# Kernel optimization log

Hardware: AMD Instinct MI355X
Metric: run time of the kernel (lower is better)

Reference implementation:

```python
import jax, jax.numpy as jnp
import numpy as np
from jax.scipy.special import logsumexp

B, DK, N, M = 16, 512, 1024, 1024
SINKHORN_ITERS = 5
EPS = 1e-8


def setup_inputs() -> dict:
    key = jax.random.key(0)
    k1, k2, k3, k4, k5 = jax.random.split(key, 5)
    return {
        "src_embedding": jax.random.normal(k1, (B, DK, N), dtype=jnp.float32),
        "tgt_embedding": jax.random.normal(k2, (B, DK, M), dtype=jnp.float32),
        "src": jax.random.normal(k3, (B, 3, N), dtype=jnp.float32),
        "tgt": jax.random.normal(k4, (B, 3, M), dtype=jnp.float32),
        # temperature must be positive; uniform in [0.05, 1.0)
        "temperature": jax.random.uniform(k5, (B,), dtype=jnp.float32, minval=0.05, maxval=1.0),
    }


def sinkhorn(scores, n_iters):
    # ZeroPad2d((0,1,0,1)): pad one slack row and one slack column with zeros
    scores = jnp.pad(scores, ((0, 0), (0, 1), (0, 1)))
    for _ in range(n_iters):
        # row normalization (all rows except slack row)
        top = scores[:, :-1, :] - logsumexp(scores[:, :-1, :], axis=2, keepdims=True)
        scores = jnp.concatenate([top, scores[:, -1:, :]], axis=1)
        # column normalization (all cols except slack col)
        left = scores[:, :, :-1] - logsumexp(scores[:, :, :-1], axis=1, keepdims=True)
        scores = jnp.concatenate([left, scores[:, :, -1:]], axis=2)
    return scores[:, :-1, :-1]


def reference(src_embedding, tgt_embedding, src, tgt, temperature):
    b, d_k, n = src_embedding.shape
    # [B, N, M] similarity scores
    dists = jnp.einsum('bdn,bdm->bnm', src_embedding, tgt_embedding) / jnp.sqrt(jnp.float32(d_k))
    affinity = dists / temperature[:, None, None]
    log_perm = sinkhorn(affinity, SINKHORN_ITERS)
    perm = jnp.exp(log_perm)                                             # [B,N,M]
    perm_norm = perm / (jnp.sum(perm, axis=2, keepdims=True) + EPS)      # [B,N,M]
    # soft correspondence: weighted_tgt[b,:,i] = sum_j perm_norm[b,i,j] * tgt[b,:,j]
    weighted_tgt = jnp.einsum('bdm,bnm->bdn', tgt, perm_norm)            # [B,3,N]
    weights = jnp.sum(perm, axis=-1, keepdims=True)                      # [B,N,1]
    weights_norm = weights / (jnp.sum(weights, axis=1, keepdims=True) + EPS)
    weights_norm = jnp.swapaxes(weights_norm, 1, 2)                      # [B,1,N]
    src_centroid = jnp.sum(src * weights_norm, axis=2, keepdims=True)    # [B,3,1]
    tgt_centroid = jnp.sum(weighted_tgt * weights_norm, axis=2, keepdims=True)
    src_centered = src - src_centroid
    corr_centered = (weighted_tgt - tgt_centroid) * weights_norm
    # weighted cross-covariance, batched 3x3
    H = jnp.einsum('bin,bjn->bij', src_centered, corr_centered)          # [B,3,3]
    # batched Procrustes via SVD (torch.svd: H = u diag(s) v^T; jnp: H = u diag(s) vh)
    u, s, vh = jnp.linalg.svd(H)
    v = jnp.swapaxes(vh, 1, 2)
    ut = jnp.swapaxes(u, 1, 2)
    r = jnp.matmul(v, ut)
    r_det = jnp.linalg.det(r)                                            # [B]
    diag = jnp.stack([jnp.ones_like(r_det), jnp.ones_like(r_det), r_det], axis=-1)  # [B,3]
    R = jnp.matmul(v * diag[:, None, :], ut)                             # [B,3,3]
    t = (jnp.matmul(-R, src_centroid) + tgt_centroid).reshape(b, 3)
    return R, t, perm_norm
```

## Files before the change

kernel.cpp:

```cpp
#include <hip/hip_runtime.h>
#include <math.h>

#define BB 16
#define NN 1024
#define MM 1024
#define DKK 512
#define CHUNKS 16

typedef short short8 __attribute__((ext_vector_type(8)));
typedef float f32x4 __attribute__((ext_vector_type(4)));

__device__ float g_u[BB*NN];
__device__ float g_v[BB*MM];
__device__ float g_w[BB*NN];
__device__ float g_wt[BB*3*NN];
__device__ float g_pm[BB*CHUNKS*MM];
__device__ float g_ps[BB*CHUNKS*MM];
__device__ __attribute__((aligned(16))) unsigned short gAh[BB*NN*DKK];
__device__ __attribute__((aligned(16))) unsigned short gAl[BB*NN*DKK];
__device__ __attribute__((aligned(16))) unsigned short gBh[BB*MM*DKK];
__device__ __attribute__((aligned(16))) unsigned short gBl[BB*MM*DKK];

__global__ __launch_bounds__(256) void zero_v_kernel() {
    int i = blockIdx.x*256 + threadIdx.x;
    if (i < BB*MM) g_v[i] = 0.0f;
}

__device__ __forceinline__ unsigned int bf16_rne(float x){
    unsigned int u = __float_as_uint(x);
    return (u + 0x7fffu + ((u>>16)&1u)) >> 16;
}

__global__ __launch_bounds__(256) void convert_split(const float* __restrict__ X,
                                                     int which) {
    unsigned short* Hh = which ? gBh : gAh;
    unsigned short* Hl = which ? gBl : gAl;
    int b  = blockIdx.z;
    int d0 = blockIdx.y * 64;
    int i0 = blockIdx.x * 64;
    __shared__ float T[64*65];
    const float* Xb = X + ((size_t)b*DKK + d0)*NN + i0;
    int t = threadIdx.x;
#pragma unroll
    for (int it=0; it<4; ++it){
        int lin = t + 256*it;
        int d = lin >> 4;
        int i4 = lin & 15;
        float4 v = *(const float4*)(Xb + (size_t)d*NN + i4*4);
        T[(i4*4+0)*65 + d] = v.x;
        T[(i4*4+1)*65 + d] = v.y;
        T[(i4*4+2)*65 + d] = v.z;
        T[(i4*4+3)*65 + d] = v.w;
    }
    __syncthreads();
    size_t obase = ((size_t)b*NN + i0)*DKK + d0;
#pragma unroll
    for (int it=0; it<2; ++it){
        int c = t + 256*it;
        int i = c >> 3;
        int p = c & 7;
        unsigned int hw[4], lw[4];
#pragma unroll
        for (int j=0;j<4;j++){
            float x0 = T[i*65 + p*8 + 2*j];
            float x1 = T[i*65 + p*8 + 2*j+1];
            unsigned int h0 = bf16_rne(x0);
            unsigned int h1 = bf16_rne(x1);
            float hf0 = __uint_as_float(h0<<16);
            float hf1 = __uint_as_float(h1<<16);
            unsigned int l0 = bf16_rne(x0 - hf0);
            unsigned int l1 = bf16_rne(x1 - hf1);
            hw[j] = h0 | (h1<<16);
            lw[j] = l0 | (l1<<16);
        }
        size_t eo = obase + (size_t)i*DKK + p*8;
        uint4 hv; hv.x=hw[0]; hv.y=hw[1]; hv.z=hw[2]; hv.w=hw[3];
        uint4 lv; lv.x=lw[0]; lv.y=lw[1]; lv.z=lw[2]; lv.w=lw[3];
        *(uint4*)(Hh + eo) = hv;
        *(uint4*)(Hl + eo) = lv;
    }
}

__global__ __launch_bounds__(256) void gemm_mfma(const float* __restrict__ temp,
                                                 float* __restrict__ C) {
    int b  = blockIdx.z;
    int i0 = blockIdx.y * 128;
    int j0 = blockIdx.x * 128;
    __shared__ __attribute__((aligned(16))) char lds[40960];
    int t = threadIdx.x;
    int lane = t & 63, w = t >> 6;
    int wr = w >> 1, wc = w & 1;
    const size_t eb = (size_t)b * NN * DKK;
    const uint4* pAh = (const uint4*)(gAh + eb);
    const uint4* pAl = (const uint4*)(gAl + eb);
    const uint4* pBh = (const uint4*)(gBh + eb);
    const uint4* pBl = (const uint4*)(gBl + eb);
    int rr = t >> 2, pp = t & 3;

    f32x4 acc[16];
#pragma unroll
    for (int q=0;q<16;q++) acc[q] = (f32x4){0.f,0.f,0.f,0.f};

    uint4 ra0, ra1, la0, la1, rb0, rb1, lb0, lb1;
    auto loadk = [&](int k0){
        int kq = k0 >> 3;
        ra0 = pAh[(size_t)(i0+rr)*64 + kq + pp];
        ra1 = pAh[(size_t)(i0+rr+64)*64 + kq + pp];
        la0 = pAl[(size_t)(i0+rr)*64 + kq + pp];
        la1 = pAl[(size_t)(i0+rr+64)*64 + kq + pp];
        rb0 = pBh[(size_t)(j0+rr)*64 + kq + pp];
        rb1 = pBh[(size_t)(j0+rr+64)*64 + kq + pp];
        lb0 = pBl[(size_t)(j0+rr)*64 + kq + pp];
        lb1 = pBl[(size_t)(j0+rr+64)*64 + kq + pp];
    };
    loadk(0);

    const char* fa = lds + (wr*64 + (lane&15))*80 + (lane>>4)*16;
    const char* fb = lds + 20480 + (wc*64 + (lane&15))*80 + (lane>>4)*16;
    char* wbase = lds + rr*80 + pp*16;

    for (int ks=0; ks<16; ++ks){
        __syncthreads();
        *(uint4*)(wbase + 0)     = ra0;
        *(uint4*)(wbase + 5120)  = ra1;
        *(uint4*)(wbase + 10240) = la0;
        *(uint4*)(wbase + 15360) = la1;
        *(uint4*)(wbase + 20480) = rb0;
        *(uint4*)(wbase + 25600) = rb1;
        *(uint4*)(wbase + 30720) = lb0;
        *(uint4*)(wbase + 35840) = lb1;
        __syncthreads();
        if (ks+1 < 16) loadk((ks+1)*32);

        short8 ah[4], al[4];
#pragma unroll
        for (int mf=0;mf<4;mf++){
            ah[mf] = *(const short8*)(fa + mf*1280);
            al[mf] = *(const short8*)(fa + 10240 + mf*1280);
        }
#pragma unroll
        for (int nf=0;nf<4;nf++){
            short8 bh = *(const short8*)(fb + nf*1280);
            short8 bl = *(const short8*)(fb + 10240 + nf*1280);
#pragma unroll
            for (int mf=0;mf<4;mf++){
                acc[mf*4+nf] = __builtin_amdgcn_mfma_f32_16x16x32_bf16(ah[mf], bh, acc[mf*4+nf], 0,0,0);
                acc[mf*4+nf] = __builtin_amdgcn_mfma_f32_16x16x32_bf16(ah[mf], bl, acc[mf*4+nf], 0,0,0);
                acc[mf*4+nf] = __builtin_amdgcn_mfma_f32_16x16x32_bf16(al[mf], bh, acc[mf*4+nf], 0,0,0);
            }
        }
    }

    float scale = 1.0f/(22.62741699796952f * temp[b]);
    float* Cb = C + ((size_t)b<<20);
    int r0c = i0 + wr*64 + ((lane>>4)<<2);
    int c0c = j0 + wc*64 + (lane&15);
#pragma unroll
    for (int mf=0;mf<4;mf++){
#pragma unroll
        for (int r2=0;r2<4;r2++){
            float* rowp = Cb + (size_t)(r0c + mf*16 + r2)*MM + c0c;
#pragma unroll
            for (int nf=0;nf<4;nf++)
                rowp[nf*16] = acc[mf*4+nf][r2]*scale;
        }
    }
}

__global__ __launch_bounds__(256) void row_lse(const float* __restrict__ S) {
    int row  = blockIdx.x*4 + (threadIdx.x>>6);
    int lane = threadIdx.x & 63;
    int b = row >> 10;
    const float4* srow = (const float4*)(S + (size_t)row*MM);
    const float4* vb   = (const float4*)(g_v + (b<<10));
    float x[16];
#pragma unroll
    for (int k=0;k<4;k++){
        float4 s4 = srow[lane + 64*k];
        float4 v4 = vb[lane + 64*k];
        x[4*k+0]=s4.x-v4.x; x[4*k+1]=s4.y-v4.y; x[4*k+2]=s4.z-v4.z; x[4*k+3]=s4.w-v4.w;
    }
    float m = x[0];
#pragma unroll
    for (int k=1;k<16;k++) m = fmaxf(m, x[k]);
    float s = 0.0f;
#pragma unroll
    for (int k=0;k<16;k++) s += __expf(x[k]-m);
    for (int off=32; off; off>>=1){
        float om = __shfl_xor(m, off);
        float os = __shfl_xor(s, off);
        float nm = fmaxf(m, om);
        s = s*__expf(m-nm) + os*__expf(om-nm);
        m = nm;
    }
    float nm = fmaxf(m, 0.0f);
    s = s*__expf(m-nm) + __expf(-nm);
    if (lane==0) g_u[row] = nm + __logf(s);
}

__global__ __launch_bounds__(256) void col_lse_partial(const float* __restrict__ S) {
    int b = blockIdx.z;
    int j = blockIdx.x*256 + threadIdx.x;
    int chunk = blockIdx.y;
    const int RC = NN/CHUNKS;
    int r0 = chunk*RC;
    const float* Sb = S + ((size_t)b*NN + r0)*MM;
    const float* ub = g_u + b*NN + r0;
    float m[4], s[4];
#pragma unroll
    for (int r=0;r<4;r++){ m[r]=-INFINITY; s[r]=0.0f; }
    for (int i=0;i<RC;i+=4){
#pragma unroll
        for (int r=0;r<4;r++){
            float x = Sb[(size_t)(i+r)*MM + j] - ub[i+r];
            float nm = fmaxf(m[r], x);
            s[r] = s[r]*__expf(m[r]-nm) + __expf(x-nm);
            m[r] = nm;
        }
    }
    float M = m[0], Ss = s[0];
#pragma unroll
    for (int r=1;r<4;r++){
        float nm = fmaxf(M, m[r]);
        Ss = Ss*__expf(M-nm) + s[r]*__expf(m[r]-nm);
        M = nm;
    }
    g_pm[(b*CHUNKS+chunk)*MM + j] = M;
    g_ps[(b*CHUNKS+chunk)*MM + j] = Ss;
}

__global__ __launch_bounds__(256) void col_lse_combine() {
    int idx = blockIdx.x*256 + threadIdx.x;
    int b = idx >> 10; int j = idx & (MM-1);
    float m = -INFINITY, s = 0.0f;
    for (int c=0;c<CHUNKS;c++){
        float om = g_pm[(b*CHUNKS+c)*MM + j];
        float os = g_ps[(b*CHUNKS+c)*MM + j];
        float nm = fmaxf(m, om);
        s = s*__expf(m-nm) + os*__expf(om-nm);
        m = nm;
    }
    float nm = fmaxf(m, 0.0f);
    s = s*__expf(m-nm) + __expf(-nm);
    g_v[idx] = nm + __logf(s);
}

__global__ __launch_bounds__(256) void finalize_rows(float* __restrict__ S,
                                                     const float* __restrict__ tgt) {
    int row  = blockIdx.x*4 + (threadIdx.x>>6);
    int lane = threadIdx.x & 63;
    int b = row >> 10;
    int i = row & (NN-1);
    float ui = g_u[row];
    float4* srow = (float4*)(S + (size_t)row*MM);
    const float4* vb = (const float4*)(g_v + (b<<10));
    const float4* t0 = (const float4*)(tgt + (size_t)b*3*MM);
    const float4* t1 = (const float4*)(tgt + (size_t)b*3*MM + MM);
    const float4* t2 = (const float4*)(tgt + (size_t)b*3*MM + 2*MM);
    float p[16];
    float rs=0.f, a0=0.f, a1=0.f, a2=0.f;
#pragma unroll
    for (int k=0;k<4;k++){
        float4 s4 = srow[lane + 64*k];
        float4 v4 = vb[lane + 64*k];
        p[4*k+0] = __expf(s4.x - ui - v4.x);
        p[4*k+1] = __expf(s4.y - ui - v4.y);
        p[4*k+2] = __expf(s4.z - ui - v4.z);
        p[4*k+3] = __expf(s4.w - ui - v4.w);
        rs += p[4*k+0]+p[4*k+1]+p[4*k+2]+p[4*k+3];
        float4 w0 = t0[lane + 64*k];
        float4 w1 = t1[lane + 64*k];
        float4 w2 = t2[lane + 64*k];
        a0 += p[4*k+0]*w0.x + p[4*k+1]*w0.y + p[4*k+2]*w0.z + p[4*k+3]*w0.w;
        a1 += p[4*k+0]*w1.x + p[4*k+1]*w1.y + p[4*k+2]*w1.z + p[4*k+3]*w1.w;
        a2 += p[4*k+0]*w2.x + p[4*k+1]*w2.y + p[4*k+2]*w2.z + p[4*k+3]*w2.w;
    }
    for (int off=32; off; off>>=1){
        rs += __shfl_xor(rs, off);
        a0 += __shfl_xor(a0, off);
        a1 += __shfl_xor(a1, off);
        a2 += __shfl_xor(a2, off);
    }
    float inv = 1.0f/(rs + 1e-8f);
#pragma unroll
    for (int k=0;k<4;k++){
        srow[lane + 64*k] = make_float4(p[4*k+0]*inv, p[4*k+1]*inv, p[4*k+2]*inv, p[4*k+3]*inv);
    }
    if (lane==0){
        g_w[row] = rs;
        g_wt[(b*3+0)*NN + i] = a0*inv;
        g_wt[(b*3+1)*NN + i] = a1*inv;
        g_wt[(b*3+2)*NN + i] = a2*inv;
    }
}

__global__ __launch_bounds__(256) void procrustes(const float* __restrict__ src,
                                                  float* __restrict__ out) {
    int b = blockIdx.x;
    int t = threadIdx.x;
    __shared__ float red[256];
    auto bsum = [&](float v)->float{
        red[t]=v; __syncthreads();
        for (int o=128;o>0;o>>=1){ if(t<o) red[t]+=red[t+o]; __syncthreads(); }
        float r=red[0]; __syncthreads(); return r;
    };
    const float* wrow = g_w + b*NN;
    float pw=0.f;
    for (int i=t;i<NN;i+=256) pw += wrow[i];
    float W = bsum(pw);
    float winv = 1.0f/(W + 1e-8f);
    const float* sb  = src  + (size_t)b*3*NN;
    const float* wtb = g_wt + (size_t)b*3*NN;
    float sc[3], tc[3];
    for (int c=0;c<3;c++){
        float p1=0.f,p2=0.f;
        for (int i=t;i<NN;i+=256){
            float wn = wrow[i]*winv;
            p1 += sb[c*NN+i]*wn;
            p2 += wtb[c*NN+i]*wn;
        }
        sc[c]=bsum(p1);
        tc[c]=bsum(p2);
    }
    float H[9];
    for (int c=0;c<3;c++)
        for (int d=0;d<3;d++){
            float p=0.f;
            for (int i=t;i<NN;i+=256){
                float wn = wrow[i]*winv;
                p += (sb[c*NN+i]-sc[c]) * ((wtb[d*NN+i]-tc[d])*wn);
            }
            H[c*3+d]=bsum(p);
        }
    if (t==0){
        double Hd[3][3];
        for (int r2=0;r2<3;r2++) for (int c2=0;c2<3;c2++) Hd[r2][c2]=H[r2*3+c2];
        double K[3][3];
        for (int i2=0;i2<3;i2++)
            for (int j2=0;j2<3;j2++){
                double acc=0;
                for (int r2=0;r2<3;r2++) acc += Hd[r2][i2]*Hd[r2][j2];
                K[i2][j2]=acc;
            }
        double V[3][3]={{1,0,0},{0,1,0},{0,0,1}};
        const int PQ[3][2]={{0,1},{0,2},{1,2}};
        for (int sweep=0; sweep<30; ++sweep){
            double off = fabs(K[0][1])+fabs(K[0][2])+fabs(K[1][2]);
            if (off < 1e-26) break;
            for (int pi=0; pi<3; ++pi){
                int p = PQ[pi][0], q = PQ[pi][1];
                double apq = K[p][q];
                if (fabs(apq) < 1e-300) continue;
                double tau = (K[q][q]-K[p][p])/(2.0*apq);
                double tt  = (tau>=0.0?1.0:-1.0)/(fabs(tau)+sqrt(1.0+tau*tau));
                double c   = 1.0/sqrt(1.0+tt*tt);
                double s   = tt*c;
                double Kpp=K[p][p], Kqq=K[q][q];
                K[p][p] = Kpp - tt*apq;
                K[q][q] = Kqq + tt*apq;
                K[p][q] = 0.0; K[q][p] = 0.0;
                int r2 = 3-p-q;
                double Krp=K[r2][p], Krq=K[r2][q];
                K[r2][p] = c*Krp - s*Krq; K[p][r2]=K[r2][p];
                K[r2][q] = s*Krp + c*Krq; K[q][r2]=K[r2][q];
                for (int rr=0; rr<3; ++rr){
                    double vp=V[rr][p], vq=V[rr][q];
                    V[rr][p] = c*vp - s*vq;
                    V[rr][q] = s*vp + c*vq;
                }
            }
        }
        double lam[3]={K[0][0],K[1][1],K[2][2]};
        int o0=0,o1=1,o2=2,tmp;
        if (lam[o0]<lam[o1]){tmp=o0;o0=o1;o1=tmp;}
        if (lam[o0]<lam[o2]){tmp=o0;o0=o2;o2=tmp;}
        if (lam[o1]<lam[o2]){tmp=o1;o1=o2;o2=tmp;}
        int ord[3]={o0,o1,o2};
        double Vs[3][3], U[3][3];
        for (int k=0;k<3;k++)
            for (int r2=0;r2<3;r2++) Vs[r2][k]=V[r2][ord[k]];
        for (int k=0;k<3;k++){
            double ux = Hd[0][0]*Vs[0][k] + Hd[0][1]*Vs[1][k] + Hd[0][2]*Vs[2][k];
            double uy = Hd[1][0]*Vs[0][k] + Hd[1][1]*Vs[1][k] + Hd[1][2]*Vs[2][k];
            double uz = Hd[2][0]*Vs[0][k] + Hd[2][1]*Vs[1][k] + Hd[2][2]*Vs[2][k];
            double n = sqrt(ux*ux+uy*uy+uz*uz);
            if (n > 1e-30){ U[0][k]=ux/n; U[1][k]=uy/n; U[2][k]=uz/n; }
            else {
                double cx = U[1][0]*U[2][1]-U[2][0]*U[1][1];
                double cy = U[2][0]*U[0][1]-U[0][0]*U[2][1];
                double cz = U[0][0]*U[1][1]-U[1][0]*U[0][1];
                U[0][k]=cx; U[1][k]=cy; U[2][k]=cz;
            }
        }
        double rm[3][3];
        for (int i2=0;i2<3;i2++)
            for (int j2=0;j2<3;j2++)
                rm[i2][j2] = Vs[i2][0]*U[j2][0] + Vs[i2][1]*U[j2][1] + Vs[i2][2]*U[j2][2];
        double det = rm[0][0]*(rm[1][1]*rm[2][2]-rm[1][2]*rm[2][1])
                   - rm[0][1]*(rm[1][0]*rm[2][2]-rm[1][2]*rm[2][0])
                   + rm[0][2]*(rm[1][0]*rm[2][1]-rm[1][1]*rm[2][0]);
        double R[3][3];
        for (int i2=0;i2<3;i2++)
            for (int j2=0;j2<3;j2++)
                R[i2][j2] = Vs[i2][0]*U[j2][0] + Vs[i2][1]*U[j2][1] + det*Vs[i2][2]*U[j2][2];
        double tv[3];
        for (int i2=0;i2<3;i2++)
            tv[i2] = -(R[i2][0]*sc[0]+R[i2][1]*sc[1]+R[i2][2]*sc[2]) + tc[i2];
        for (int i2=0;i2<3;i2++)
            for (int j2=0;j2<3;j2++)
                out[b*9 + i2*3 + j2] = (float)R[i2][j2];
        for (int i2=0;i2<3;i2++)
            out[144 + b*3 + i2] = (float)tv[i2];
    }
}

extern "C" void kernel_launch(void* const* d_in, const int* in_sizes, int n_in,
                              void* d_out, int out_size, void* d_ws, size_t ws_size,
                              hipStream_t stream) {
    const float* src_emb = (const float*)d_in[0];
    const float* tgt_emb = (const float*)d_in[1];
    const float* src     = (const float*)d_in[2];
    const float* tgt     = (const float*)d_in[3];
    const float* temp    = (const float*)d_in[4];
    float* out = (float*)d_out;
    float* S = out + 192;

    hipLaunchKernelGGL(zero_v_kernel, dim3(64), dim3(256), 0, stream);
    hipLaunchKernelGGL(convert_split, dim3(16,8,16), dim3(256), 0, stream, src_emb, 0);
    hipLaunchKernelGGL(convert_split, dim3(16,8,16), dim3(256), 0, stream, tgt_emb, 1);
    hipLaunchKernelGGL(gemm_mfma, dim3(8,8,16), dim3(256), 0, stream, temp, S);
    for (int it=0; it<5; ++it){
        hipLaunchKernelGGL(row_lse, dim3(4096), dim3(256), 0, stream, S);
        hipLaunchKernelGGL(col_lse_partial, dim3(4,CHUNKS,16), dim3(256), 0, stream, S);
        hipLaunchKernelGGL(col_lse_combine, dim3(64), dim3(256), 0, stream);
    }
    hipLaunchKernelGGL(finalize_rows, dim3(4096), dim3(256), 0, stream, S, tgt);
    hipLaunchKernelGGL(procrustes, dim3(16), dim3(256), 0, stream, src, out);
}
```

Before: 408.1 us.

## Fuse row and column LSE passes into one Sinkhorn kernel; remap GEMM blocks per XCD

Replaces the separate row_lse and col_lse_partial kernels with a single sink_iter kernel. It loads a 16-row block of S into LDS once, computes the row log-sum-exp, then produces per-block column partial max/sum from the same LDS copy. This cuts each iteration from two full reads of the 64 MB score matrix to one. The cost is many more column partials (64 per batch instead of 16) for the combine kernel to reduce, plus a large LDS footprint per block that limits occupancy. Separately, the GEMM grid is flattened and remapped so each XCD handles two whole batches, aiming for better L2 locality.

```diff
diff --git a/kernel.cpp b/kernel.cpp
--- a/kernel.cpp
+++ b/kernel.cpp
@@ -5,7 +5,8 @@
 #define NN 1024
 #define MM 1024
 #define DKK 512
-#define CHUNKS 16
+#define RBLK 16
+#define NRB  (NN/RBLK)
 
 typedef short short8 __attribute__((ext_vector_type(8)));
 typedef float f32x4 __attribute__((ext_vector_type(4)));
@@ -14,8 +15,8 @@
 __device__ float g_v[BB*MM];
 __device__ float g_w[BB*NN];
 __device__ float g_wt[BB*3*NN];
-__device__ float g_pm[BB*CHUNKS*MM];
-__device__ float g_ps[BB*CHUNKS*MM];
+__device__ float g_pm[BB*NRB*MM];
+__device__ float g_ps[BB*NRB*MM];
 __device__ __attribute__((aligned(16))) unsigned short gAh[BB*NN*DKK];
 __device__ __attribute__((aligned(16))) unsigned short gAl[BB*NN*DKK];
 __device__ __attribute__((aligned(16))) unsigned short gBh[BB*MM*DKK];
@@ -83,9 +84,13 @@
 
 __global__ __launch_bounds__(256) void gemm_mfma(const float* __restrict__ temp,
                                                  float* __restrict__ C) {
-    int b  = blockIdx.z;
-    int i0 = blockIdx.y * 128;
-    int j0 = blockIdx.x * 128;
+    int id   = blockIdx.x;
+    int xcd  = id & 7;
+    int slot = id >> 3;
+    int b    = xcd*2 + (slot >> 6);
+    int sub  = slot & 63;
+    int i0   = (sub >> 3) << 7;
+    int j0   = (sub & 7) << 7;
     __shared__ __attribute__((aligned(16))) char lds[40960];
     int t = threadIdx.x;
     int lane = t & 63, w = t >> 6;
@@ -167,75 +172,82 @@
     }
 }
 
-__global__ __launch_bounds__(256) void row_lse(const float* __restrict__ S) {
-    int row  = blockIdx.x*4 + (threadIdx.x>>6);
-    int lane = threadIdx.x & 63;
-    int b = row >> 10;
-    const float4* srow = (const float4*)(S + (size_t)row*MM);
-    const float4* vb   = (const float4*)(g_v + (b<<10));
-    float x[16];
-#pragma unroll
-    for (int k=0;k<4;k++){
-        float4 s4 = srow[lane + 64*k];
-        float4 v4 = vb[lane + 64*k];
-        x[4*k+0]=s4.x-v4.x; x[4*k+1]=s4.y-v4.y; x[4*k+2]=s4.z-v4.z; x[4*k+3]=s4.w-v4.w;
-    }
-    float m = x[0];
-#pragma unroll
-    for (int k=1;k<16;k++) m = fmaxf(m, x[k]);
-    float s = 0.0f;
-#pragma unroll
-    for (int k=0;k<16;k++) s += __expf(x[k]-m);
-    for (int off=32; off; off>>=1){
-        float om = __shfl_xor(m, off);
-        float os = __shfl_xor(s, off);
-        float nm = fmaxf(m, om);
-        s = s*__expf(m-nm) + os*__expf(om-nm);
-        m = nm;
-    }
-    float nm = fmaxf(m, 0.0f);
-    s = s*__expf(m-nm) + __expf(-nm);
-    if (lane==0) g_u[row] = nm + __logf(s);
-}
-
-__global__ __launch_bounds__(256) void col_lse_partial(const float* __restrict__ S) {
-    int b = blockIdx.z;
-    int j = blockIdx.x*256 + threadIdx.x;
-    int chunk = blockIdx.y;
-    const int RC = NN/CHUNKS;
-    int r0 = chunk*RC;
-    const float* Sb = S + ((size_t)b*NN + r0)*MM;
-    const float* ub = g_u + b*NN + r0;
-    float m[4], s[4];
-#pragma unroll
-    for (int r=0;r<4;r++){ m[r]=-INFINITY; s[r]=0.0f; }
-    for (int i=0;i<RC;i+=4){
-#pragma unroll
-        for (int r=0;r<4;r++){
-            float x = Sb[(size_t)(i+r)*MM + j] - ub[i+r];
-            float nm = fmaxf(m[r], x);
-            s[r] = s[r]*__expf(m[r]-nm) + __expf(x-nm);
-            m[r] = nm;
-        }
-    }
-    float M = m[0], Ss = s[0];
-#pragma unroll
-    for (int r=1;r<4;r++){
-        float nm = fmaxf(M, m[r]);
-        Ss = Ss*__expf(M-nm) + s[r]*__expf(m[r]-nm);
-        M = nm;
-    }
-    g_pm[(b*CHUNKS+chunk)*MM + j] = M;
-    g_ps[(b*CHUNKS+chunk)*MM + j] = Ss;
+__global__ __launch_bounds__(256) void sink_iter(const float* __restrict__ S) {
+    int b   = blockIdx.y;
+    int rb  = blockIdx.x;
+    int row0 = rb*RBLK;
+    int t = threadIdx.x;
+    __shared__ float Ls[RBLK*1028];
+    __shared__ float v_l[1024];
+    __shared__ float u_l[RBLK];
+
+    float4 v4 = *(const float4*)(g_v + (b<<10) + t*4);
+    *(float4*)(v_l + t*4) = v4;
+
+    const float* Sb = S + ((size_t)b*NN + row0)*MM;
+#pragma unroll
+    for (int rr=0; rr<RBLK; ++rr){
+        float4 s4 = *(const float4*)(Sb + (size_t)rr*MM + t*4);
+        s4.x -= v4.x; s4.y -= v4.y; s4.z -= v4.z; s4.w -= v4.w;
+        *(float4*)(&Ls[rr*1028 + t*4]) = s4;
+    }
+    __syncthreads();
+
+    {
+        int r = t >> 4, c = t & 15;
+        const float* Lr = &Ls[r*1028 + c];
+        float m = -INFINITY;
+#pragma unroll
+        for (int k=0;k<64;k++) m = fmaxf(m, Lr[16*k]);
+#pragma unroll
+        for (int off=1; off<16; off<<=1) m = fmaxf(m, __shfl_xor(m, off));
+        m = fmaxf(m, 0.0f);
+        float s = 0.0f;
+#pragma unroll
+        for (int k=0;k<64;k++) s += __expf(Lr[16*k] - m);
+#pragma unroll
+        for (int off=1; off<16; off<<=1) s += __shfl_xor(s, off);
+        s += __expf(-m);
+        float u = m + __logf(s);
+        if (c==0){ u_l[r] = u; g_u[b*NN + row0 + r] = u; }
+    }
+    __syncthreads();
+
+    float mm[4], ss[4];
+#pragma unroll
+    for (int q=0;q<4;q++){ mm[q]=-INFINITY; ss[q]=0.f; }
+#pragma unroll
+    for (int r=0;r<RBLK;++r){
+        float ur = u_l[r];
+        const float* Lr = &Ls[r*1028];
+#pragma unroll
+        for (int q=0;q<4;q++)
+            mm[q] = fmaxf(mm[q], Lr[t + 256*q] - ur);
+    }
+#pragma unroll
+    for (int r=0;r<RBLK;++r){
+        float ur = u_l[r];
+        const float* Lr = &Ls[r*1028];
+#pragma unroll
+        for (int q=0;q<4;q++)
+            ss[q] += __expf(Lr[t + 256*q] - ur - mm[q]);
+    }
+    size_t pbase = ((size_t)(b*NRB + rb) << 10) + t;
+#pragma unroll
+    for (int q=0;q<4;q++){
+        g_pm[pbase + 256*q] = mm[q] + v_l[t + 256*q];
+        g_ps[pbase + 256*q] = ss[q];
+    }
 }
 
 __global__ __launch_bounds__(256) void col_lse_combine() {
     int idx = blockIdx.x*256 + threadIdx.x;
     int b = idx >> 10; int j = idx & (MM-1);
     float m = -INFINITY, s = 0.0f;
-    for (int c=0;c<CHUNKS;c++){
-        float om = g_pm[(b*CHUNKS+c)*MM + j];
-        float os = g_ps[(b*CHUNKS+c)*MM + j];
+    size_t base = ((size_t)(b*NRB) << 10) + j;
+    for (int c=0;c<NRB;c++){
+        float om = g_pm[base + ((size_t)c<<10)];
+        float os = g_ps[base + ((size_t)c<<10)];
         float nm = fmaxf(m, om);
         s = s*__expf(m-nm) + os*__expf(om-nm);
         m = nm;
@@ -428,10 +440,9 @@
     hipLaunchKernelGGL(zero_v_kernel, dim3(64), dim3(256), 0, stream);
     hipLaunchKernelGGL(convert_split, dim3(16,8,16), dim3(256), 0, stream, src_emb, 0);
     hipLaunchKernelGGL(convert_split, dim3(16,8,16), dim3(256), 0, stream, tgt_emb, 1);
-    hipLaunchKernelGGL(gemm_mfma, dim3(8,8,16), dim3(256), 0, stream, temp, S);
+    hipLaunchKernelGGL(gemm_mfma, dim3(1024), dim3(256), 0, stream, temp, S);
     for (int it=0; it<5; ++it){
-        hipLaunchKernelGGL(row_lse, dim3(4096), dim3(256), 0, stream, S);
-        hipLaunchKernelGGL(col_lse_partial, dim3(4,CHUNKS,16), dim3(256), 0, stream, S);
+        hipLaunchKernelGGL(sink_iter, dim3(NRB,BB), dim3(256), 0, stream, S);
         hipLaunchKernelGGL(col_lse_combine, dim3(64), dim3(256), 0, stream);
     }
     hipLaunchKernelGGL(finalize_rows, dim3(4096), dim3(256), 0, stream, S, tgt);
```

New measurement: 366.1 us. 10.3% less time.
